# Kernel tuning notes

Hardware: AMD Instinct MI355X
Metric: run time of the kernel (lower is better)

Reference implementation:

```python
import jax, jax.numpy as jnp
import numpy as np

B, N = 64, 256
DV, DP, DT, DF = 2048, 8, 768, 512


def setup_inputs() -> dict:
    key = jax.random.key(0)
    ks = jax.random.split(key, 9)
    visual = jax.random.normal(ks[0], (B, N, DV), dtype=jnp.float32)
    position = jax.random.uniform(ks[1], (B, N, DP), dtype=jnp.float32)
    text = jax.random.normal(ks[2], (B, N, DT), dtype=jnp.float32)
    s = 0.02
    Wt = jax.random.normal(ks[3], (DT, DF), dtype=jnp.float32) * s
    bt = jnp.zeros((DF,), dtype=jnp.float32)
    Wo = jax.random.normal(ks[4], (DV + DP, DF), dtype=jnp.float32) * s
    bo = jnp.zeros((DF,), dtype=jnp.float32)
    Wa = jax.random.normal(ks[5], (DF, 1), dtype=jnp.float32) * s
    ba = jnp.zeros((1,), dtype=jnp.float32)
    return {"visual": visual, "position": position, "text": text,
            "Wt": Wt, "bt": bt, "Wo": Wo, "bo": bo, "Wa": Wa, "ba": ba}


def relative_positions(position):
    # position: [B, N, P]
    n = position.shape[1]
    eye = jnp.eye(n, dtype=position.dtype)  # replaces per-element torch.diag loops
    p1 = position[:, :, None, :]            # [B, N, 1, P] -> row copies
    p2 = position[:, None, :, :]            # [B, 1, N, P] -> col copies
    p3 = eye[None, :, :, None] * p1         # diag(position[b, :, p])
    return p1 - p2 + p3                     # [B, N, N, P]


def reference(visual, position, text, Wt, bt, Wo, bo, Wa, ba):
    # query from first text token
    query = jax.nn.gelu(text[:, 0, :] @ Wt + bt, approximate=False)  # [B, DF]
    rel = relative_positions(position).sum(axis=2)                   # [B, N, P]
    objects = jnp.concatenate((visual, rel), axis=-1)                # [B, N, DV+DP]
    proj = objects @ Wo + bo                                         # [B, N, DF]
    scores = proj * query[:, None, :]                                # gated fusion
    out = (scores @ Wa + ba)[..., 0]                                 # [B, N]
    return out
```

## Files before the change

### kernel.cpp

```cpp
#include <hip/hip_runtime.h>
#include <hip/hip_bf16.h>
#include <math.h>

#define B_   64
#define N_   256
#define DV_  2048
#define DP_  8
#define DT_  768
#define DF_  512
#define DK_  2056

#define WS_WT 0
#define WS_S  32768
#define WS_C  33280
#define WS_V  33344

__global__ __launch_bounds__(256) void kA(
    const float* __restrict__ pos,
    const float* __restrict__ text,
    const float* __restrict__ Wt,
    const float* __restrict__ bt,
    const float* __restrict__ Wa,
    float* __restrict__ wT,
    float* __restrict__ S)
{
    const int b = blockIdx.x >> 2;
    const int g = blockIdx.x & 3;
    const int t = threadIdx.x;
    const int a = t & 31;
    const int kh = t >> 5;

    __shared__ float tx[DT_];
    __shared__ float4 sred[8][32];
    __shared__ float spos[32][DP_];

    for (int k = t; k < DT_; k += 256)
        tx[k] = text[(size_t)b * N_ * DT_ + k];

    if (g == 0) {
        const int d = t & 7, gi = t >> 3;
        float s = 0.f;
        for (int i = gi; i < N_; i += 32)
            s += pos[(size_t)b * N_ * DP_ + i * DP_ + d];
        spos[gi][d] = s;
    }
    __syncthreads();

    if (g == 0 && t < DP_) {
        float s = 0.f;
        #pragma unroll
        for (int gi = 0; gi < 32; ++gi) s += spos[gi][t];
        S[b * DP_ + t] = s;
    }

    const int f0 = g * 128 + 4 * a;
    float4 acc = make_float4(0.f, 0.f, 0.f, 0.f);
    const int kbase = kh * 96;
    for (int j = 0; j < 96; ++j) {
        const int k = kbase + j;
        const float x = tx[k];
        const float4 wv = *(const float4*)(Wt + (size_t)k * DF_ + f0);
        acc.x = fmaf(x, wv.x, acc.x);
        acc.y = fmaf(x, wv.y, acc.y);
        acc.z = fmaf(x, wv.z, acc.z);
        acc.w = fmaf(x, wv.w, acc.w);
    }
    sred[kh][a] = acc;
    __syncthreads();

    if (t < 32) {
        float4 s = sred[0][t];
        #pragma unroll
        for (int h = 1; h < 8; ++h) {
            const float4 p = sred[h][t];
            s.x += p.x; s.y += p.y; s.z += p.z; s.w += p.w;
        }
        const float sv[4] = {s.x, s.y, s.z, s.w};
        #pragma unroll
        for (int cc = 0; cc < 4; ++cc) {
            const int f = g * 128 + 4 * t + cc;
            const float z = sv[cc] + bt[f];
            const float ge = 0.5f * z * (1.f + erff(z * 0.70710678118654752f));
            wT[(size_t)f * B_ + b] = ge * Wa[f];
        }
    }
}

__global__ __launch_bounds__(256) void kB(
    const float* __restrict__ Wo,
    const float* __restrict__ bo,
    const float* __restrict__ ba,
    const float* __restrict__ wT,
    float* __restrict__ v,
    float* __restrict__ c)
{
    const int t = threadIdx.x;
    __shared__ float  wo[8][DF_ + 4];
    __shared__ float4 red1[8][16];
    __shared__ float  sbo[DF_];
    __shared__ float4 cred[16][16];

    if (blockIdx.x < 257) {
        const int k0 = blockIdx.x * 8;
        for (int idx = t; idx < 8 * 128; idx += 256) {
            const int row = idx >> 7, c4 = idx & 127;
            const float4 x = *(const float4*)(Wo + (size_t)(k0 + row) * DF_ + c4 * 4);
            *(float4*)(&wo[row][c4 * 4]) = x;
        }
        __syncthreads();

        const int bq = t & 15;
        const int rr = (t >> 4) & 7;
        const int hh = t >> 7;
        const float* wrow = wo[rr];
        float4 acc = make_float4(0.f, 0.f, 0.f, 0.f);
        const int fbase = hh * 256;
        for (int j = 0; j < 256; ++j) {
            const int f = fbase + j;
            const float s = wrow[f];
            const float4 wv = *(const float4*)(wT + (size_t)f * B_ + 4 * bq);
            acc.x = fmaf(s, wv.x, acc.x);
            acc.y = fmaf(s, wv.y, acc.y);
            acc.z = fmaf(s, wv.z, acc.z);
            acc.w = fmaf(s, wv.w, acc.w);
        }
        if (hh) red1[rr][bq] = acc;
        __syncthreads();
        if (!hh) {
            const float4 p = red1[rr][bq];
            acc.x += p.x; acc.y += p.y; acc.z += p.z; acc.w += p.w;
            const float av[4] = {acc.x, acc.y, acc.z, acc.w};
            #pragma unroll
            for (int cc = 0; cc < 4; ++cc)
                v[(size_t)(4 * bq + cc) * DK_ + k0 + rr] = av[cc];
        }
    } else {
        for (int k = t; k < DF_; k += 256) sbo[k] = bo[k];
        __syncthreads();
        const int bq = t & 15;
        const int fh = t >> 4;
        float4 acc = make_float4(0.f, 0.f, 0.f, 0.f);
        for (int j = 0; j < 32; ++j) {
            const int f = fh * 32 + j;
            const float s = sbo[f];
            const float4 wv = *(const float4*)(wT + (size_t)f * B_ + 4 * bq);
            acc.x = fmaf(s, wv.x, acc.x);
            acc.y = fmaf(s, wv.y, acc.y);
            acc.z = fmaf(s, wv.z, acc.z);
            acc.w = fmaf(s, wv.w, acc.w);
        }
        cred[fh][bq] = acc;
        __syncthreads();
        if (fh == 0) {
            float4 s = cred[0][bq];
            #pragma unroll
            for (int h = 1; h < 16; ++h) {
                const float4 p = cred[h][bq];
                s.x += p.x; s.y += p.y; s.z += p.z; s.w += p.w;
            }
            const float sv[4] = {s.x, s.y, s.z, s.w};
            #pragma unroll
            for (int cc = 0; cc < 4; ++cc)
                c[4 * bq + cc] = sv[cc] + ba[0];
        }
    }
}

__global__ __launch_bounds__(256) void kC(
    const float* __restrict__ visual,
    const float* __restrict__ pos,
    const float* __restrict__ v,
    const float* __restrict__ S,
    const float* __restrict__ c,
    float* __restrict__ out)
{
    const int t    = threadIdx.x;
    const int wave = t >> 6;
    const int lane = t & 63;
    const int R0   = blockIdx.x * 16 + wave * 4;
    const int b    = R0 >> 8;
    const int i0   = R0 & 255;

    const float4* vb = (const float4*)(v + (size_t)b * DK_);
    const float4* v0 = (const float4*)(visual + ((size_t)b * N_ + i0) * DV_);

    float a0 = 0.f, a1 = 0.f, a2 = 0.f, a3 = 0.f;
    #pragma unroll
    for (int j = 0; j < 8; ++j) {
        const int idx = lane + 64 * j;
        const float4 wv = vb[idx];
        const float4 x0 = v0[idx];
        const float4 x1 = v0[idx + 512];
        const float4 x2 = v0[idx + 1024];
        const float4 x3 = v0[idx + 1536];
        a0 = fmaf(x0.x, wv.x, a0); a0 = fmaf(x0.y, wv.y, a0);
        a0 = fmaf(x0.z, wv.z, a0); a0 = fmaf(x0.w, wv.w, a0);
        a1 = fmaf(x1.x, wv.x, a1); a1 = fmaf(x1.y, wv.y, a1);
        a1 = fmaf(x1.z, wv.z, a1); a1 = fmaf(x1.w, wv.w, a1);
        a2 = fmaf(x2.x, wv.x, a2); a2 = fmaf(x2.y, wv.y, a2);
        a2 = fmaf(x2.z, wv.z, a2); a2 = fmaf(x2.w, wv.w, a2);
        a3 = fmaf(x3.x, wv.x, a3); a3 = fmaf(x3.y, wv.y, a3);
        a3 = fmaf(x3.z, wv.z, a3); a3 = fmaf(x3.w, wv.w, a3);
    }
    #pragma unroll
    for (int off = 1; off < 64; off <<= 1) {
        a0 += __shfl_xor(a0, off, 64);
        a1 += __shfl_xor(a1, off, 64);
        a2 += __shfl_xor(a2, off, 64);
        a3 += __shfl_xor(a3, off, 64);
    }

    if (lane < 4) {
        const float accq = (lane == 0) ? a0 : (lane == 1) ? a1 : (lane == 2) ? a2 : a3;
        const int i = i0 + lane;
        const float* v2 = v + (size_t)b * DK_ + DV_;
        const float* pr = pos + ((size_t)b * N_ + i) * DP_;
        const float* Sb = S + b * DP_;
        float pd = 0.f, sd = 0.f;
        #pragma unroll
        for (int d = 0; d < DP_; ++d) {
            pd = fmaf(pr[d], v2[d], pd);
            sd = fmaf(Sb[d], v2[d], sd);
        }
        out[(size_t)b * N_ + i] = accq + 257.f * pd - sd + c[b];
    }
}

extern "C" void kernel_launch(void* const* d_in, const int* in_sizes, int n_in,
                              void* d_out, int out_size, void* d_ws, size_t ws_size,
                              hipStream_t stream) {
    const float* visual   = (const float*)d_in[0];
    const float* position = (const float*)d_in[1];
    const float* text     = (const float*)d_in[2];
    const float* Wt       = (const float*)d_in[3];
    const float* bt       = (const float*)d_in[4];
    const float* Wo       = (const float*)d_in[5];
    const float* bo       = (const float*)d_in[6];
    const float* Wa       = (const float*)d_in[7];
    const float* ba       = (const float*)d_in[8];
    float* out = (float*)d_out;

    float* ws = (float*)d_ws;
    float* wT = ws + WS_WT;
    float* S  = ws + WS_S;
    float* c  = ws + WS_C;
    float* v  = ws + WS_V;

    kA<<<256, 256, 0, stream>>>(position, text, Wt, bt, Wa, wT, S);
    kB<<<258, 256, 0, stream>>>(Wo, bo, ba, wT, v, c);
    kC<<<(B_ * N_) / 16, 256, 0, stream>>>(visual, position, v, S, c, out);
}
```

Before: 55.70 us.

## Retile all three kernels for more blocks and better register reuse

kA now assigns each block four batches by a 32-wide feature slice, so every Wt load is reused across four batch rows, and the K reduction is split 32 ways. kB handles four Wo rows per block over 514 blocks, reusing each wT load across four rows, and reduces over sixteen feature groups. kC drops from four rows per wave to two and launches twice as many blocks to raise parallelism on the dominant visual streaming pass. The cost is more blocks, more shared-memory reduction work and less per-thread reuse of the v vector in kC.

```diff
diff --git a/kernel.cpp b/kernel.cpp
--- a/kernel.cpp
+++ b/kernel.cpp
@@ -24,61 +24,75 @@
     float* __restrict__ wT,
     float* __restrict__ S)
 {
-    const int b = blockIdx.x >> 2;
-    const int g = blockIdx.x & 3;
-    const int t = threadIdx.x;
-    const int a = t & 31;
-    const int kh = t >> 5;
-
-    __shared__ float tx[DT_];
-    __shared__ float4 sred[8][32];
-    __shared__ float spos[32][DP_];
-
-    for (int k = t; k < DT_; k += 256)
-        tx[k] = text[(size_t)b * N_ * DT_ + k];
-
-    if (g == 0) {
-        const int d = t & 7, gi = t >> 3;
+    const int bq = blockIdx.x >> 4;
+    const int fg = blockIdx.x & 15;
+    const int t  = threadIdx.x;
+
+    __shared__ float  tx[4][DT_];
+    __shared__ float4 sred[4][32][8];
+    __shared__ float  spos[4][8][DP_];
+
+    #pragma unroll
+    for (int bb = 0; bb < 4; ++bb)
+        for (int k = t; k < DT_; k += 256)
+            tx[bb][k] = text[(size_t)(bq * 4 + bb) * N_ * DT_ + k];
+
+    if (fg == 0) {
+        const int bb = t >> 6, lane = t & 63;
+        const int d = lane & 7, g8 = lane >> 3;
         float s = 0.f;
-        for (int i = gi; i < N_; i += 32)
-            s += pos[(size_t)b * N_ * DP_ + i * DP_ + d];
-        spos[gi][d] = s;
+        for (int i = g8; i < N_; i += 8)
+            s += pos[(size_t)(bq * 4 + bb) * N_ * DP_ + i * DP_ + d];
+        spos[bb][g8][d] = s;
     }
     __syncthreads();
 
-    if (g == 0 && t < DP_) {
+    if (fg == 0 && t < 32) {
+        const int bb = t >> 3, d = t & 7;
         float s = 0.f;
         #pragma unroll
-        for (int gi = 0; gi < 32; ++gi) s += spos[gi][t];
-        S[b * DP_ + t] = s;
-    }
-
-    const int f0 = g * 128 + 4 * a;
-    float4 acc = make_float4(0.f, 0.f, 0.f, 0.f);
-    const int kbase = kh * 96;
-    for (int j = 0; j < 96; ++j) {
+        for (int g = 0; g < 8; ++g) s += spos[bb][g][d];
+        S[(bq * 4 + bb) * DP_ + d] = s;
+    }
+
+    const int fq = t & 7;
+    const int kc = t >> 3;
+    const int f0 = fg * 32 + fq * 4;
+    float4 a0 = make_float4(0.f, 0.f, 0.f, 0.f);
+    float4 a1 = a0, a2 = a0, a3 = a0;
+    const int kbase = kc * 24;
+    #pragma unroll 4
+    for (int j = 0; j < 24; ++j) {
         const int k = kbase + j;
-        const float x = tx[k];
         const float4 wv = *(const float4*)(Wt + (size_t)k * DF_ + f0);
-        acc.x = fmaf(x, wv.x, acc.x);
-        acc.y = fmaf(x, wv.y, acc.y);
-        acc.z = fmaf(x, wv.z, acc.z);
-        acc.w = fmaf(x, wv.w, acc.w);
-    }
-    sred[kh][a] = acc;
+        const float x0 = tx[0][k], x1 = tx[1][k], x2 = tx[2][k], x3 = tx[3][k];
+        a0.x = fmaf(x0, wv.x, a0.x); a0.y = fmaf(x0, wv.y, a0.y);
+        a0.z = fmaf(x0, wv.z, a0.z); a0.w = fmaf(x0, wv.w, a0.w);
+        a1.x = fmaf(x1, wv.x, a1.x); a1.y = fmaf(x1, wv.y, a1.y);
+        a1.z = fmaf(x1, wv.z, a1.z); a1.w = fmaf(x1, wv.w, a1.w);
+        a2.x = fmaf(x2, wv.x, a2.x); a2.y = fmaf(x2, wv.y, a2.y);
+        a2.z = fmaf(x2, wv.z, a2.z); a2.w = fmaf(x2, wv.w, a2.w);
+        a3.x = fmaf(x3, wv.x, a3.x); a3.y = fmaf(x3, wv.y, a3.y);
+        a3.z = fmaf(x3, wv.z, a3.z); a3.w = fmaf(x3, wv.w, a3.w);
+    }
+    sred[0][kc][fq] = a0;
+    sred[1][kc][fq] = a1;
+    sred[2][kc][fq] = a2;
+    sred[3][kc][fq] = a3;
     __syncthreads();
 
     if (t < 32) {
-        float4 s = sred[0][t];
-        #pragma unroll
-        for (int h = 1; h < 8; ++h) {
-            const float4 p = sred[h][t];
+        const int bb = t >> 3, fq2 = t & 7;
+        float4 s = sred[bb][0][fq2];
+        for (int k2 = 1; k2 < 32; ++k2) {
+            const float4 p = sred[bb][k2][fq2];
             s.x += p.x; s.y += p.y; s.z += p.z; s.w += p.w;
         }
         const float sv[4] = {s.x, s.y, s.z, s.w};
+        const int b = bq * 4 + bb;
         #pragma unroll
         for (int cc = 0; cc < 4; ++cc) {
-            const int f = g * 128 + 4 * t + cc;
+            const int f = fg * 32 + fq2 * 4 + cc;
             const float z = sv[cc] + bt[f];
             const float ge = 0.5f * z * (1.f + erff(z * 0.70710678118654752f));
             wT[(size_t)f * B_ + b] = ge * Wa[f];
@@ -95,44 +109,57 @@
     float* __restrict__ c)
 {
     const int t = threadIdx.x;
-    __shared__ float  wo[8][DF_ + 4];
-    __shared__ float4 red1[8][16];
+    __shared__ float  wo[4][DF_];
+    __shared__ float4 red[4][16][16];
     __shared__ float  sbo[DF_];
     __shared__ float4 cred[16][16];
 
-    if (blockIdx.x < 257) {
-        const int k0 = blockIdx.x * 8;
-        for (int idx = t; idx < 8 * 128; idx += 256) {
-            const int row = idx >> 7, c4 = idx & 127;
-            const float4 x = *(const float4*)(Wo + (size_t)(k0 + row) * DF_ + c4 * 4);
-            *(float4*)(&wo[row][c4 * 4]) = x;
+    if (blockIdx.x < 514) {
+        const int k0 = blockIdx.x * 4;
+        {
+            const float4* src = (const float4*)(Wo + (size_t)k0 * DF_);
+            float4*       dst = (float4*)wo;
+            dst[t]       = src[t];
+            dst[t + 256] = src[t + 256];
         }
         __syncthreads();
 
         const int bq = t & 15;
-        const int rr = (t >> 4) & 7;
-        const int hh = t >> 7;
-        const float* wrow = wo[rr];
-        float4 acc = make_float4(0.f, 0.f, 0.f, 0.f);
-        const int fbase = hh * 256;
-        for (int j = 0; j < 256; ++j) {
+        const int fg = t >> 4;
+        float4 acc0 = make_float4(0.f, 0.f, 0.f, 0.f);
+        float4 acc1 = acc0, acc2 = acc0, acc3 = acc0;
+        const int fbase = fg * 32;
+        #pragma unroll 4
+        for (int j = 0; j < 32; ++j) {
             const int f = fbase + j;
-            const float s = wrow[f];
             const float4 wv = *(const float4*)(wT + (size_t)f * B_ + 4 * bq);
-            acc.x = fmaf(s, wv.x, acc.x);
-            acc.y = fmaf(s, wv.y, acc.y);
-            acc.z = fmaf(s, wv.z, acc.z);
-            acc.w = fmaf(s, wv.w, acc.w);
-        }
-        if (hh) red1[rr][bq] = acc;
-        __syncthreads();
-        if (!hh) {
-            const float4 p = red1[rr][bq];
-            acc.x += p.x; acc.y += p.y; acc.z += p.z; acc.w += p.w;
-            const float av[4] = {acc.x, acc.y, acc.z, acc.w};
+            const float s0 = wo[0][f], s1 = wo[1][f], s2 = wo[2][f], s3 = wo[3][f];
+            acc0.x = fmaf(s0, wv.x, acc0.x); acc0.y = fmaf(s0, wv.y, acc0.y);
+            acc0.z = fmaf(s0, wv.z, acc0.z); acc0.w = fmaf(s0, wv.w, acc0.w);
+            acc1.x = fmaf(s1, wv.x, acc1.x); acc1.y = fmaf(s1, wv.y, acc1.y);
+            acc1.z = fmaf(s1, wv.z, acc1.z); acc1.w = fmaf(s1, wv.w, acc1.w);
+            acc2.x = fmaf(s2, wv.x, acc2.x); acc2.y = fmaf(s2, wv.y, acc2.y);
+            acc2.z = fmaf(s2, wv.z, acc2.z); acc2.w = fmaf(s2, wv.w, acc2.w);
+            acc3.x = fmaf(s3, wv.x, acc3.x); acc3.y = fmaf(s3, wv.y, acc3.y);
+            acc3.z = fmaf(s3, wv.z, acc3.z); acc3.w = fmaf(s3, wv.w, acc3.w);
+        }
+        red[0][fg][bq] = acc0;
+        red[1][fg][bq] = acc1;
+        red[2][fg][bq] = acc2;
+        red[3][fg][bq] = acc3;
+        __syncthreads();
+        if (t < 64) {
+            const int r = t >> 4, bq2 = t & 15;
+            float4 s = red[r][0][bq2];
+            #pragma unroll
+            for (int g = 1; g < 16; ++g) {
+                const float4 p = red[r][g][bq2];
+                s.x += p.x; s.y += p.y; s.z += p.z; s.w += p.w;
+            }
+            const float sv[4] = {s.x, s.y, s.z, s.w};
             #pragma unroll
             for (int cc = 0; cc < 4; ++cc)
-                v[(size_t)(4 * bq + cc) * DK_ + k0 + rr] = av[cc];
+                v[(size_t)(4 * bq2 + cc) * DK_ + k0 + r] = sv[cc];
         }
     } else {
         for (int k = t; k < DF_; k += 256) sbo[k] = bo[k];
@@ -177,41 +204,33 @@
     const int t    = threadIdx.x;
     const int wave = t >> 6;
     const int lane = t & 63;
-    const int R0   = blockIdx.x * 16 + wave * 4;
+    const int R0   = blockIdx.x * 8 + wave * 2;
     const int b    = R0 >> 8;
     const int i0   = R0 & 255;
 
     const float4* vb = (const float4*)(v + (size_t)b * DK_);
     const float4* v0 = (const float4*)(visual + ((size_t)b * N_ + i0) * DV_);
 
-    float a0 = 0.f, a1 = 0.f, a2 = 0.f, a3 = 0.f;
+    float a0 = 0.f, a1 = 0.f;
     #pragma unroll
     for (int j = 0; j < 8; ++j) {
         const int idx = lane + 64 * j;
         const float4 wv = vb[idx];
         const float4 x0 = v0[idx];
         const float4 x1 = v0[idx + 512];
-        const float4 x2 = v0[idx + 1024];
-        const float4 x3 = v0[idx + 1536];
         a0 = fmaf(x0.x, wv.x, a0); a0 = fmaf(x0.y, wv.y, a0);
         a0 = fmaf(x0.z, wv.z, a0); a0 = fmaf(x0.w, wv.w, a0);
         a1 = fmaf(x1.x, wv.x, a1); a1 = fmaf(x1.y, wv.y, a1);
         a1 = fmaf(x1.z, wv.z, a1); a1 = fmaf(x1.w, wv.w, a1);
-        a2 = fmaf(x2.x, wv.x, a2); a2 = fmaf(x2.y, wv.y, a2);
-        a2 = fmaf(x2.z, wv.z, a2); a2 = fmaf(x2.w, wv.w, a2);
-        a3 = fmaf(x3.x, wv.x, a3); a3 = fmaf(x3.y, wv.y, a3);
-        a3 = fmaf(x3.z, wv.z, a3); a3 = fmaf(x3.w, wv.w, a3);
     }
     #pragma unroll
     for (int off = 1; off < 64; off <<= 1) {
         a0 += __shfl_xor(a0, off, 64);
         a1 += __shfl_xor(a1, off, 64);
-        a2 += __shfl_xor(a2, off, 64);
-        a3 += __shfl_xor(a3, off, 64);
-    }
-
-    if (lane < 4) {
-        const float accq = (lane == 0) ? a0 : (lane == 1) ? a1 : (lane == 2) ? a2 : a3;
+    }
+
+    if (lane < 2) {
+        const float accq = (lane == 0) ? a0 : a1;
         const int i = i0 + lane;
         const float* v2 = v + (size_t)b * DK_ + DV_;
         const float* pr = pos + ((size_t)b * N_ + i) * DP_;
@@ -247,6 +266,6 @@
     float* v  = ws + WS_V;
 
     kA<<<256, 256, 0, stream>>>(position, text, Wt, bt, Wa, wT, S);
-    kB<<<258, 256, 0, stream>>>(Wo, bo, ba, wT, v, c);
-    kC<<<(B_ * N_) / 16, 256, 0, stream>>>(visual, position, v, S, c, out);
-}
+    kB<<<515, 256, 0, stream>>>(Wo, bo, ba, wT, v, c);
+    kC<<<2048, 256, 0, stream>>>(visual, position, v, S, c, out);
+}
```

Result: faster. 49.72 us (-10.7%).
